# Kernel tuning notes

Hardware: AMD Instinct MI355X
Metric: run time of the kernel (lower is better)

## Reference

```python
import jax, jax.numpy as jnp
import numpy as np

B, N, R = 2, 64, 16
D = 64      # node_dim_in
H = 256     # hidden_dim
EOUT = 64   # edge_dim_out
PSTEP = 2


def _lin_init(key, fi, fo):
    k1, k2 = jax.random.split(key)
    s = 1.0 / np.sqrt(fi)
    W = jax.random.uniform(k1, (fi, fo), minval=-s, maxval=s, dtype=jnp.float32)
    b = jax.random.uniform(k2, (fo,), minval=-s, maxval=s, dtype=jnp.float32)
    return W, b


def setup_inputs() -> dict:
    key = jax.random.key(0)
    ks = jax.random.split(key, 11)
    node_rep = jax.random.normal(ks[0], (B, N, R, D), dtype=jnp.float32)
    ne_W, ne_b = _lin_init(ks[1], D, H)          # node_encoder
    ee_W, ee_b = _lin_init(ks[2], 2 * D, H)      # edge_encoder (edge_rep is None)
    np_W1, np_b1 = _lin_init(ks[3], 3 * H, H)    # node_propagator
    np_W2, np_b2 = _lin_init(ks[4], H, H)
    ep0_W1, ep0_b1 = _lin_init(ks[5], 3 * H, H)  # edge_propagators[0]
    ep0_W2, ep0_b2 = _lin_init(ks[6], H, H)
    ep1_W1, ep1_b1 = _lin_init(ks[7], 3 * H, H)  # edge_propagators[1]
    ep1_W2, ep1_b2 = _lin_init(ks[8], H, H)
    pr_W1, pr_b1 = _lin_init(ks[9], 2 * H, H)    # edge_predictor
    pr_W2, pr_b2 = _lin_init(ks[10], H, EOUT)
    return dict(node_rep=node_rep, ne_W=ne_W, ne_b=ne_b, ee_W=ee_W, ee_b=ee_b,
                np_W1=np_W1, np_b1=np_b1, np_W2=np_W2, np_b2=np_b2,
                ep0_W1=ep0_W1, ep0_b1=ep0_b1, ep0_W2=ep0_W2, ep0_b2=ep0_b2,
                ep1_W1=ep1_W1, ep1_b1=ep1_b1, ep1_W2=ep1_W2, ep1_b2=ep1_b2,
                pr_W1=pr_W1, pr_b1=pr_b1, pr_W2=pr_W2, pr_b2=pr_b2)


def _propnet(node_rep, ne_W, ne_b, ee_W, ee_b, np_W1, np_b1, np_W2, np_b2,
             ep_params, pr_W1, pr_b1, pr_W2, pr_b2):
    relu = jax.nn.relu
    # node encoder: [B,N,R,H]
    node_enc = relu(node_rep @ ne_W + ne_b)
    # edge encoder on cat(node_rep_r, node_rep_s): split the weight instead of
    # materializing the [B,N,N,R,2D] repeated-concat tensor (same math).
    # receiver varies over axis 1, sender over axis 2.
    edge_enc = relu(node_rep[:, :, None] @ ee_W[:D]
                    + node_rep[:, None, :] @ ee_W[D:] + ee_b)  # [B,N,N,R,H]
    node_effect = node_enc
    edge_effect = edge_enc
    for (W1, b1, W2, b2) in ep_params:
        # edge propagator on cat(effect_r, effect_s, edge_effect)
        h = relu(node_effect[:, :, None] @ W1[:H]
                 + node_effect[:, None, :] @ W1[H:2 * H]
                 + edge_effect @ W1[2 * H:] + b1)
        edge_effect = relu(h @ W2 + b2)                 # [B,N,N,R,H]
        agg = edge_effect.sum(axis=2)                   # sum over senders -> [B,N,R,H]
        g = relu(node_enc @ np_W1[:H]
                 + node_effect @ np_W1[H:2 * H]
                 + agg @ np_W1[2 * H:] + np_b1)
        node_effect = relu(g @ np_W2 + np_b2)
    # edge predictor on cat(edge_effect, edge_enc) -> split weight
    p = relu(edge_effect @ pr_W1[:H] + edge_enc @ pr_W1[H:] + pr_b1)
    edge_pred = p @ pr_W2 + pr_b2                       # [B,N,N,R,EOUT]
    return edge_pred


def reference(node_rep, ne_W, ne_b, ee_W, ee_b, np_W1, np_b1, np_W2, np_b2,
              ep0_W1, ep0_b1, ep0_W2, ep0_b2, ep1_W1, ep1_b1, ep1_W2, ep1_b2,
              pr_W1, pr_b1, pr_W2, pr_b2):
    ep_params = [(ep0_W1, ep0_b1, ep0_W2, ep0_b2), (ep1_W1, ep1_b1, ep1_W2, ep1_b2)]
    return _propnet(node_rep, ne_W, ne_b, ee_W, ee_b, np_W1, np_b1, np_W2, np_b2,
                    ep_params, pr_W1, pr_b1, pr_W2, pr_b2)
```

## Files before the change

### kernel.cpp

```cpp
#include <hip/hip_runtime.h>
#include <hip/hip_bf16.h>


typedef __attribute__((ext_vector_type(8))) short short8;
typedef __attribute__((ext_vector_type(4))) float f32x4;
typedef __attribute__((ext_vector_type(2))) unsigned int u32x2;

#define DI __device__ __forceinline__

constexpr size_t WF_SZ = 131072;
constexpr size_t OFF_NEW  = 14 * WF_SZ;
constexpr size_t OFF_EE1  = OFF_NEW + 32768;
constexpr size_t OFF_EE2  = OFF_EE1 + 32768;
constexpr size_t OFF_PW2  = OFF_EE2 + 32768;
constexpr size_t OFF_NENC = OFF_PW2 + 32768;
constexpr size_t OFF_X1   = OFF_NENC + (size_t)2048 * 256 * 2;
constexpr size_t SM = (size_t)2048 * 256 * 4;
constexpr size_t OFF_X2   = OFF_X1 + SM;
constexpr size_t OFF_E1   = OFF_X2 + SM;
constexpr size_t OFF_E2I  = OFF_E1 + SM;
constexpr size_t OFF_NE1  = OFF_E2I + 32 * 32768;
constexpr size_t OFF_AGG  = OFF_NE1 + SM;
constexpr size_t OFF_IMG  = OFF_AGG + 2 * SM;

DI unsigned short f2bf(float f) {
    unsigned u = __builtin_bit_cast(unsigned, f);
    u += 0x7fffu + ((u >> 16) & 1u);
    return (unsigned short)(u >> 16);
}
DI float bf2f(unsigned short s) {
    unsigned u = (unsigned)s << 16;
    return __builtin_bit_cast(float, u);
}

DI int kmap(int g, int e) { return 4 * g + (e & 3) + ((e >> 2) << 4); }

DI void dma16(const void* g, void* l) {
    __builtin_amdgcn_global_load_lds((const __attribute__((address_space(1))) void*)g,
                                     (__attribute__((address_space(3))) void*)l, 16, 0, 0);
}

__global__ __launch_bounds__(64) void kconv(const float* ep0W1, const float* ep0W2,
                                            const float* ep1W1, const float* ep1W2,
                                            const float* prW1, const float* prW2,
                                            const float* npW1, const float* npW2,
                                            const float* neW, const float* eeW,
                                            unsigned short* wsu)
{
    int bid = blockIdx.x, l = threadIdx.x;
    const float* src; unsigned short* dst; int NT = 16, ld = 256, f;
    if (bid < 1792) {
        int m = bid >> 7; f = bid & 127;
        switch (m) {
            case 0:  src = ep0W1 + 512 * 256; break;
            case 1:  src = ep0W2;             break;
            case 2:  src = ep1W1 + 512 * 256; break;
            case 3:  src = ep1W2;             break;
            case 4:  src = prW1;              break;
            case 5:  src = prW1 + 256 * 256;  break;
            case 6:  src = ep0W1;             break;
            case 7:  src = ep0W1 + 256 * 256; break;
            case 8:  src = npW1 + 256 * 256;  break;
            case 9:  src = npW1 + 512 * 256;  break;
            case 10: src = npW1;              break;
            case 11: src = npW2;              break;
            case 12: src = ep1W1;             break;
            default: src = ep1W1 + 256 * 256; break;
        }
        dst = wsu + (size_t)m * (WF_SZ / 2);
    } else if (bid < 1888) {
        int m = (bid - 1792) >> 5; f = (bid - 1792) & 31;
        src = (m == 0) ? neW : (m == 1) ? eeW : eeW + 64 * 256;
        dst = wsu + ((m == 0) ? OFF_NEW : (m == 1) ? OFF_EE1 : OFF_EE2) / 2;
    } else {
        f = bid - 1888; NT = 4; ld = 64; src = prW2; dst = wsu + OFF_PW2 / 2;
    }
    int kt = f / NT, nt = f % NT;
    int g = l >> 4, c = nt * 16 + (l & 15);
    unsigned short* o = dst + (size_t)((kt * NT + nt) * 64 + l) * 8;
#pragma unroll
    for (int e = 0; e < 8; ++e) {
        int k = 32 * kt + kmap(g, e);
        o[e] = f2bf(src[(size_t)k * ld + c]);
    }
}

template <int LDB>
DI short8 load_afrag(const unsigned char* lds, int row, int kt, int g) {
    int sw = (row & 7) << 4;
    int kb = 64 * kt + 8 * g;
    union { short8 s; u32x2 u[2]; } u_;
    u_.u[0] = *(const u32x2*)(lds + row * LDB + (kb ^ sw));
    u_.u[1] = *(const u32x2*)(lds + row * LDB + ((kb + 32) ^ sw));
    return u_.s;
}

template <int MI>
DI void zero_acc(f32x4 (&acc)[MI][4]) {
#pragma unroll
    for (int mi = 0; mi < MI; ++mi)
#pragma unroll
        for (int ni = 0; ni < 4; ++ni) acc[mi][ni] = (f32x4){0.f, 0.f, 0.f, 0.f};
}

template <int MI, int KT, int LDB>
DI void gemm_tile(const unsigned char* lds, const unsigned short* Wf,
                  f32x4 (&acc)[MI][4], int wv, int l) {
    const int g = l >> 4, l15 = l & 15;
    for (int kt = 0; kt < KT; ++kt) {
        short8 af[MI];
#pragma unroll
        for (int mi = 0; mi < MI; ++mi) af[mi] = load_afrag<LDB>(lds, 16 * mi + l15, kt, g);
        short8 bf[4];
#pragma unroll
        for (int ni = 0; ni < 4; ++ni)
            bf[ni] = *(const short8*)(Wf + (size_t)((kt * 16 + 4 * wv + ni) * 64 + l) * 8);
#pragma unroll
        for (int ni = 0; ni < 4; ++ni)
#pragma unroll
            for (int mi = 0; mi < MI; ++mi)
                acc[mi][ni] = __builtin_amdgcn_mfma_f32_16x16x32_bf16(af[mi], bf[ni], acc[mi][ni], 0, 0, 0);
    }
}

template <int MI>
DI void store_tile_f32(float* dst, int r0, f32x4 (&acc)[MI][4], int wv, int l) {
    int g = l >> 4, l15 = l & 15;
#pragma unroll
    for (int ni = 0; ni < 4; ++ni) {
        int col = 64 * wv + 16 * ni + l15;
#pragma unroll
        for (int mi = 0; mi < MI; ++mi)
#pragma unroll
            for (int q = 0; q < 4; ++q)
                dst[(size_t)(r0 + 16 * mi + 4 * g + q) * 256 + col] = acc[mi][ni][q];
    }
}

template <int MI>
DI void store_tile_bias(float* dst, const float* bias, int r0, f32x4 (&acc)[MI][4], int wv, int l) {
    int g = l >> 4, l15 = l & 15;
#pragma unroll
    for (int ni = 0; ni < 4; ++ni) {
        int col = 64 * wv + 16 * ni + l15;
        float bb = bias[col];
#pragma unroll
        for (int mi = 0; mi < MI; ++mi)
#pragma unroll
            for (int q = 0; q < 4; ++q)
                dst[(size_t)(r0 + 16 * mi + 4 * g + q) * 256 + col] = acc[mi][ni][q] + bb;
    }
}

template <int MI>
DI void store_E2img(unsigned char* E2img, int r0, f32x4 (&acc)[MI][4], int wv, int l) {
    int g = l >> 4, l15 = l & 15;
#pragma unroll
    for (int ni = 0; ni < 4; ++ni) {
        int col = 64 * wv + 16 * ni + l15;
#pragma unroll
        for (int mi = 0; mi < MI; ++mi)
#pragma unroll
            for (int q = 0; q < 4; ++q) {
                int nr = r0 + 16 * mi + 4 * g + q;
                int b = nr >> 10, j = (nr >> 4) & 63, r = nr & 15;
                size_t byte = (size_t)(b * 16 + r) * 32768 + ((j * 512 + col * 2) ^ ((j & 7) << 4));
                *(unsigned short*)(E2img + byte) = f2bf(acc[mi][ni][q]);
            }
    }
}

__global__ __launch_bounds__(256) void knode12(const float* node_rep, const float* neb,
        const float* ep0b1,
        const unsigned short* neWf, const unsigned short* eeW1f, const unsigned short* eeW2f,
        const unsigned short* E1wf, const unsigned short* E2wf, const unsigned short* NE1wf,
        unsigned short* node_enc, float* X1, float* X2, float* E1b, unsigned char* E2img, float* NE1)
{
    __shared__ __align__(16) unsigned char ldsA[32 * 128];
    __shared__ __align__(16) unsigned char ldsB[32 * 512];
    const int r0 = blockIdx.x * 32, tid = threadIdx.x;
    {
        int row = tid >> 3, c0 = (tid & 7) * 8;
        const float* src = node_rep + (size_t)(r0 + row) * 64 + c0;
        union { short8 s; unsigned short u[8]; } v;
#pragma unroll
        for (int e = 0; e < 8; ++e) v.u[e] = f2bf(src[e]);
        *(short8*)&ldsA[row * 128 + ((c0 * 2) ^ ((row & 7) << 4))] = v.s;
    }
    __syncthreads();
    const int l = tid & 63, wv = tid >> 6, g = l >> 4, l15 = l & 15;
    f32x4 acc[2][4];
    zero_acc(acc);
    gemm_tile<2, 2, 128>(ldsA, neWf, acc, wv, l);
#pragma unroll
    for (int ni = 0; ni < 4; ++ni) {
        int col = 64 * wv + 16 * ni + l15;
        float bb = neb[col];
#pragma unroll
        for (int mi = 0; mi < 2; ++mi)
#pragma unroll
            for (int q = 0; q < 4; ++q) {
                int row = 16 * mi + 4 * g + q;
                unsigned short bv = f2bf(fmaxf(acc[mi][ni][q] + bb, 0.f));
                *(unsigned short*)&ldsB[row * 512 + ((col * 2) ^ ((row & 7) << 4))] = bv;
                node_enc[(size_t)(r0 + row) * 256 + col] = bv;
            }
    }
    zero_acc(acc);
    gemm_tile<2, 2, 128>(ldsA, eeW1f, acc, wv, l);
    store_tile_f32<2>(X1, r0, acc, wv, l);
    zero_acc(acc);
    gemm_tile<2, 2, 128>(ldsA, eeW2f, acc, wv, l);
    store_tile_f32<2>(X2, r0, acc, wv, l);
    __syncthreads();
    zero_acc(acc);
    gemm_tile<2, 8, 512>(ldsB, E1wf, acc, wv, l);
    store_tile_bias<2>(E1b, ep0b1, r0, acc, wv, l);
    zero_acc(acc);
    gemm_tile<2, 8, 512>(ldsB, E2wf, acc, wv, l);
    store_E2img<2>(E2img, r0, acc, wv, l);
    zero_acc(acc);
    gemm_tile<2, 8, 512>(ldsB, NE1wf, acc, wv, l);
    store_tile_f32<2>(NE1, r0, acc, wv, l);
}

__global__ __launch_bounds__(256) void knode3(const unsigned short* node_enc, const float* agg,
        const float* NE1, const float* npb1, const float* npb2, const float* ep1b1,
        const unsigned short* NE2wf, const unsigned short* NAGGwf, const unsigned short* npW2f,
        const unsigned short* ep1Awf, const unsigned short* ep1Bwf,
        float* E1b, unsigned char* E2img)
{
    __shared__ __align__(16) unsigned char ldsA[32 * 512];
    __shared__ __align__(16) unsigned char ldsB[32 * 512];
    const int r0 = blockIdx.x * 32, tid = threadIdx.x;
    {
        int row = tid >> 3, cbase = (tid & 7) * 32;
        int sw = (row & 7) << 4;
#pragma unroll
        for (int cc = 0; cc < 2; ++cc) {
            int c0 = cbase + cc * 16;
            short8 lo = *(const short8*)(node_enc + (size_t)(r0 + row) * 256 + c0);
            short8 hi = *(const short8*)(node_enc + (size_t)(r0 + row) * 256 + c0 + 8);
            *(short8*)&ldsA[row * 512 + ((c0 * 2) ^ sw)] = lo;
            *(short8*)&ldsA[row * 512 + ((c0 * 2 + 16) ^ sw)] = hi;
            union { short8 s; unsigned short u[8]; } v0, v1;
            const float* aA = agg + (size_t)(r0 + row) * 256 + c0;
            const float* aB = aA + (size_t)2048 * 256;
#pragma unroll
            for (int e = 0; e < 8; ++e) {
                v0.u[e] = f2bf(aA[e] + aB[e]);
                v1.u[e] = f2bf(aA[8 + e] + aB[8 + e]);
            }
            *(short8*)&ldsB[row * 512 + ((c0 * 2) ^ sw)] = v0.s;
            *(short8*)&ldsB[row * 512 + ((c0 * 2 + 16) ^ sw)] = v1.s;
        }
    }
    __syncthreads();
    const int l = tid & 63, wv = tid >> 6, g = l >> 4, l15 = l & 15;
    f32x4 acc[2][4];
    zero_acc(acc);
    gemm_tile<2, 8, 512>(ldsA, NE2wf, acc, wv, l);
    gemm_tile<2, 8, 512>(ldsB, NAGGwf, acc, wv, l);
    __syncthreads();
#pragma unroll
    for (int ni = 0; ni < 4; ++ni) {
        int col = 64 * wv + 16 * ni + l15;
        float bb = npb1[col];
#pragma unroll
        for (int mi = 0; mi < 2; ++mi)
#pragma unroll
            for (int q = 0; q < 4; ++q) {
                int row = 16 * mi + 4 * g + q;
                float v = fmaxf(acc[mi][ni][q] + NE1[(size_t)(r0 + row) * 256 + col] + bb, 0.f);
                *(unsigned short*)&ldsA[row * 512 + ((col * 2) ^ ((row & 7) << 4))] = f2bf(v);
            }
    }
    __syncthreads();
    zero_acc(acc);
    gemm_tile<2, 8, 512>(ldsA, npW2f, acc, wv, l);
    __syncthreads();
#pragma unroll
    for (int ni = 0; ni < 4; ++ni) {
        int col = 64 * wv + 16 * ni + l15;
        float bb = npb2[col];
#pragma unroll
        for (int mi = 0; mi < 2; ++mi)
#pragma unroll
            for (int q = 0; q < 4; ++q) {
                int row = 16 * mi + 4 * g + q;
                *(unsigned short*)&ldsB[row * 512 + ((col * 2) ^ ((row & 7) << 4))] =
                    f2bf(fmaxf(acc[mi][ni][q] + bb, 0.f));
            }
    }
    __syncthreads();
    zero_acc(acc);
    gemm_tile<2, 8, 512>(ldsB, ep1Awf, acc, wv, l);
    store_tile_bias<2>(E1b, ep1b1, r0, acc, wv, l);
    zero_acc(acc);
    gemm_tile<2, 8, 512>(ldsB, ep1Bwf, acc, wv, l);
    store_E2img<2>(E2img, r0, acc, wv, l);
}

__global__ __launch_bounds__(256, 2) void kstep1(const float* X1, const float* X2, const float* eeb,
                                                 const float* E1b, const unsigned char* E2img,
                                                 const float* b2,
                                                 const unsigned short* WfA, const unsigned short* WfB,
                                                 unsigned char* img, float* agg)
{
    __shared__ __align__(16) unsigned char T[32 * 512];
    __shared__ __align__(16) unsigned char L2e[32 * 512];
    const int bb = blockIdx.x, tid = threadIdx.x;
    const int bir = bb >> 1, half = bb & 1;
    const int b = bir >> 10, r = bir & 15;
    const int l = tid & 63, wv = tid >> 6, g = l >> 4, l15 = l & 15;

    {
        const unsigned char* src = E2img + (size_t)(b * 16 + r) * 32768 + (size_t)half * 16384;
#pragma unroll
        for (int p = 0; p < 4; ++p) {
            int chunk = wv * 4 + p;
            dma16(src + chunk * 1024 + l * 16, &L2e[chunk * 1024]);
        }
    }
    {
        int rlo = tid >> 5;
        int c0 = (tid & 31) * 8;
        for (int p = 0; p < 4; ++p) {
            int row = p * 8 + rlo;
            union { short8 s; unsigned short u[8]; } v;
            int nrj = b * 1024 + (half * 32 + row) * 16 + r;
#pragma unroll
            for (int e = 0; e < 8; ++e) {
                float x = X1[(size_t)bir * 256 + c0 + e] + X2[(size_t)nrj * 256 + c0 + e] + eeb[c0 + e];
                v.u[e] = f2bf(fmaxf(x, 0.f));
            }
            *(short8*)&T[row * 512 + ((c0 * 2) ^ ((row & 7) << 4))] = v.s;
        }
    }
    __syncthreads();

    f32x4 acc[2][4];
    zero_acc(acc);
    gemm_tile<2, 8, 512>(T, WfA, acc, wv, l);
    __syncthreads();
#pragma unroll
    for (int ni = 0; ni < 4; ++ni) {
        int col = 64 * wv + 16 * ni + l15;
        float e1b = E1b[(size_t)bir * 256 + col];
#pragma unroll
        for (int mi = 0; mi < 2; ++mi)
#pragma unroll
            for (int q = 0; q < 4; ++q) {
                int row = 16 * mi + 4 * g + q;
                float e2 = bf2f(*(const unsigned short*)&L2e[row * 512 + ((col * 2) ^ ((row & 7) << 4))]);
                float h = fmaxf(acc[mi][ni][q] + e1b + e2, 0.f);
                *(unsigned short*)&T[row * 512 + ((col * 2) ^ ((row & 7) << 4))] = f2bf(h);
                acc[mi][ni][q] = 0.f;
            }
    }
    __syncthreads();
    gemm_tile<2, 8, 512>(T, WfB, acc, wv, l);
    unsigned short* out16 = (unsigned short*)(img + (size_t)bb * 16384);
#pragma unroll
    for (int ni = 0; ni < 4; ++ni) {
        int col = 64 * wv + 16 * ni + l15;
        float bb2 = b2[col];
        float s = 0.f;
#pragma unroll
        for (int mi = 0; mi < 2; ++mi)
#pragma unroll
            for (int q = 0; q < 4; ++q) {
                int row = 16 * mi + 4 * g + q;
                float e = fmaxf(acc[mi][ni][q] + bb2, 0.f);
                out16[(row * 512 + ((col * 2) ^ ((row & 7) << 4))) >> 1] = f2bf(e);
                s += e;
            }
        s += __shfl_xor(s, 16);
        s += __shfl_xor(s, 32);
        if (l < 16) agg[((size_t)half * 2048 + bir) * 256 + 64 * wv + 16 * ni + l] = s;
    }
}

__global__ __launch_bounds__(256, 2) void kstep2pred(const float* X1, const float* X2, const float* eeb,
        const float* E1b, const unsigned char* E2img, const float* b2,
        const unsigned short* WfA, const unsigned short* WfB,
        const unsigned short* WfPA, const unsigned short* WfPB, const unsigned short* WfP2,
        const float* prb1, const float* prb2,
        const unsigned char* img, float* out)
{
    __shared__ __align__(16) unsigned char T[32 * 512];
    __shared__ __align__(16) unsigned char L2e[32 * 512];
    const int bb = blockIdx.x, tid = threadIdx.x;
    const int bir = bb >> 1, half = bb & 1;
    const int b = bir >> 10, r = bir & 15;
    const int ebase = (bir >> 4) * 1024 + r;
    const int l = tid & 63, wv = tid >> 6, g = l >> 4, l15 = l & 15;

    {
        const unsigned char* src = img + (size_t)bb * 16384;
        const unsigned char* srcE = E2img + (size_t)(b * 16 + r) * 32768 + (size_t)half * 16384;
#pragma unroll
        for (int p = 0; p < 4; ++p) {
            int chunk = wv * 4 + p;
            dma16(src + chunk * 1024 + l * 16, &T[chunk * 1024]);
            dma16(srcE + chunk * 1024 + l * 16, &L2e[chunk * 1024]);
        }
    }
    __syncthreads();

    f32x4 acc[2][4];
    zero_acc(acc);
    gemm_tile<2, 8, 512>(T, WfA, acc, wv, l);
    __syncthreads();
#pragma unroll
    for (int ni = 0; ni < 4; ++ni) {
        int col = 64 * wv + 16 * ni + l15;
        float e1b = E1b[(size_t)bir * 256 + col];
#pragma unroll
        for (int mi = 0; mi < 2; ++mi)
#pragma unroll
            for (int q = 0; q < 4; ++q) {
                int row = 16 * mi + 4 * g + q;
                float e2 = bf2f(*(const unsigned short*)&L2e[row * 512 + ((col * 2) ^ ((row & 7) << 4))]);
                float h = fmaxf(acc[mi][ni][q] + e1b + e2, 0.f);
                *(unsigned short*)&T[row * 512 + ((col * 2) ^ ((row & 7) << 4))] = f2bf(h);
                acc[mi][ni][q] = 0.f;
            }
    }
    __syncthreads();
    gemm_tile<2, 8, 512>(T, WfB, acc, wv, l);
    __syncthreads();
#pragma unroll
    for (int ni = 0; ni < 4; ++ni) {
        int col = 64 * wv + 16 * ni + l15;
        float bb2 = b2[col];
#pragma unroll
        for (int mi = 0; mi < 2; ++mi)
#pragma unroll
            for (int q = 0; q < 4; ++q) {
                int row = 16 * mi + 4 * g + q;
                *(unsigned short*)&T[row * 512 + ((col * 2) ^ ((row & 7) << 4))] =
                    f2bf(fmaxf(acc[mi][ni][q] + bb2, 0.f));
            }
    }
    __syncthreads();
    zero_acc(acc);
    gemm_tile<2, 8, 512>(T, WfPA, acc, wv, l);
    __syncthreads();
    {
        int rlo = tid >> 5;
        int c0 = (tid & 31) * 8;
        for (int p = 0; p < 4; ++p) {
            int row = p * 8 + rlo;
            union { short8 s; unsigned short u[8]; } v;
            int nrj = b * 1024 + (half * 32 + row) * 16 + r;
#pragma unroll
            for (int e = 0; e < 8; ++e) {
                float x = X1[(size_t)bir * 256 + c0 + e] + X2[(size_t)nrj * 256 + c0 + e] + eeb[c0 + e];
                v.u[e] = f2bf(fmaxf(x, 0.f));
            }
            *(short8*)&T[row * 512 + ((c0 * 2) ^ ((row & 7) << 4))] = v.s;
        }
    }
    __syncthreads();
    gemm_tile<2, 8, 512>(T, WfPB, acc, wv, l);
    __syncthreads();
#pragma unroll
    for (int ni = 0; ni < 4; ++ni) {
        int col = 64 * wv + 16 * ni + l15;
        float pb = prb1[col];
#pragma unroll
        for (int mi = 0; mi < 2; ++mi)
#pragma unroll
            for (int q = 0; q < 4; ++q) {
                int row = 16 * mi + 4 * g + q;
                float p = fmaxf(acc[mi][ni][q] + pb, 0.f);
                *(unsigned short*)&T[row * 512 + ((col * 2) ^ ((row & 7) << 4))] = f2bf(p);
            }
    }
    __syncthreads();
    f32x4 acc3[2];
#pragma unroll
    for (int mi = 0; mi < 2; ++mi) acc3[mi] = (f32x4){0.f, 0.f, 0.f, 0.f};
    for (int kt = 0; kt < 8; ++kt) {
        short8 bf = *(const short8*)(WfP2 + (size_t)((kt * 4 + wv) * 64 + l) * 8);
#pragma unroll
        for (int mi = 0; mi < 2; ++mi) {
            short8 af = load_afrag<512>(T, 16 * mi + l15, kt, g);
            acc3[mi] = __builtin_amdgcn_mfma_f32_16x16x32_bf16(af, bf, acc3[mi], 0, 0, 0);
        }
    }
    int colo = 16 * wv + l15;
    float pb2 = prb2[colo];
#pragma unroll
    for (int mi = 0; mi < 2; ++mi)
#pragma unroll
        for (int q = 0; q < 4; ++q) {
            int row = 16 * mi + 4 * g + q;
            out[(size_t)(ebase + (half * 32 + row) * 16) * 64 + colo] = acc3[mi][q] + pb2;
        }
}

extern "C" void kernel_launch(void* const* d_in, const int* in_sizes, int n_in,
                              void* d_out, int out_size, void* d_ws, size_t ws_size,
                              hipStream_t stream)
{
    (void)in_sizes; (void)n_in; (void)out_size; (void)ws_size;
    const float* node_rep = (const float*)d_in[0];
    const float* neW   = (const float*)d_in[1];
    const float* neb   = (const float*)d_in[2];
    const float* eeW   = (const float*)d_in[3];
    const float* eeb   = (const float*)d_in[4];
    const float* npW1  = (const float*)d_in[5];
    const float* npb1  = (const float*)d_in[6];
    const float* npW2  = (const float*)d_in[7];
    const float* npb2  = (const float*)d_in[8];
    const float* ep0W1 = (const float*)d_in[9];
    const float* ep0b1 = (const float*)d_in[10];
    const float* ep0W2 = (const float*)d_in[11];
    const float* ep0b2 = (const float*)d_in[12];
    const float* ep1W1 = (const float*)d_in[13];
    const float* ep1b1 = (const float*)d_in[14];
    const float* ep1W2 = (const float*)d_in[15];
    const float* ep1b2 = (const float*)d_in[16];
    const float* prW1  = (const float*)d_in[17];
    const float* prb1  = (const float*)d_in[18];
    const float* prW2  = (const float*)d_in[19];
    const float* prb2  = (const float*)d_in[20];

    char* ws = (char*)d_ws;
    unsigned short* wsu = (unsigned short*)ws;
    auto wfull = [&](int i) { return (const unsigned short*)(ws + (size_t)i * WF_SZ); };
    unsigned short* node_enc = (unsigned short*)(ws + OFF_NENC);
    float* X1   = (float*)(ws + OFF_X1);
    float* X2   = (float*)(ws + OFF_X2);
    float* E1b  = (float*)(ws + OFF_E1);
    unsigned char* E2img = (unsigned char*)(ws + OFF_E2I);
    float* NE1  = (float*)(ws + OFF_NE1);
    float* agg  = (float*)(ws + OFF_AGG);
    unsigned char* img = (unsigned char*)(ws + OFF_IMG);
    const unsigned short* neWf  = (const unsigned short*)(ws + OFF_NEW);
    const unsigned short* eeW1f = (const unsigned short*)(ws + OFF_EE1);
    const unsigned short* eeW2f = (const unsigned short*)(ws + OFF_EE2);
    const unsigned short* prW2f = (const unsigned short*)(ws + OFF_PW2);

    kconv<<<dim3(1920), dim3(64), 0, stream>>>(ep0W1, ep0W2, ep1W1, ep1W2, prW1, prW2,
                                               npW1, npW2, neW, eeW, wsu);
    knode12<<<dim3(64), dim3(256), 0, stream>>>(node_rep, neb, ep0b1, neWf, eeW1f, eeW2f,
                                                wfull(6), wfull(7), wfull(10),
                                                node_enc, X1, X2, E1b, E2img, NE1);
    kstep1<<<dim3(4096), dim3(256), 0, stream>>>(X1, X2, eeb, E1b, E2img, ep0b2,
                                                 wfull(0), wfull(1), img, agg);
    knode3<<<dim3(64), dim3(256), 0, stream>>>(node_enc, agg, NE1, npb1, npb2, ep1b1,
                                               wfull(8), wfull(9), wfull(11),
                                               wfull(12), wfull(13), E1b, E2img);
    kstep2pred<<<dim3(4096), dim3(256), 0, stream>>>(X1, X2, eeb, E1b, E2img, ep1b2,
                                                     wfull(2), wfull(3), wfull(4), wfull(5),
                                                     prW2f, prb1, prb2, img, (float*)d_out);
}
```

Before: 344.5 us.

## Load sender edge term from fp32 global into registers and double-buffer LDS

The sender-side E2 projection is now kept as an fp32 row-major buffer instead of a swizzled bf16 image. The edge kernels read it directly into registers per accumulator element, with no LDS DMA staging. A second LDS buffer (U) alternates with T so several __syncthreads barriers between GEMM phases can be dropped. The cost is twice the bytes for E2, uncoalesced scattered global loads, and extra register pressure from 36 prefetched floats under a 2-blocks-per-SM launch bound.

```diff
diff --git a/kernel.cpp b/kernel.cpp
--- a/kernel.cpp
+++ b/kernel.cpp
@@ -18,8 +18,8 @@
 constexpr size_t SM = (size_t)2048 * 256 * 4;
 constexpr size_t OFF_X2   = OFF_X1 + SM;
 constexpr size_t OFF_E1   = OFF_X2 + SM;
-constexpr size_t OFF_E2I  = OFF_E1 + SM;
-constexpr size_t OFF_NE1  = OFF_E2I + 32 * 32768;
+constexpr size_t OFF_E2   = OFF_E1 + SM;
+constexpr size_t OFF_NE1  = OFF_E2 + SM;
 constexpr size_t OFF_AGG  = OFF_NE1 + SM;
 constexpr size_t OFF_IMG  = OFF_AGG + 2 * SM;
 
@@ -27,10 +27,6 @@
     unsigned u = __builtin_bit_cast(unsigned, f);
     u += 0x7fffu + ((u >> 16) & 1u);
     return (unsigned short)(u >> 16);
-}
-DI float bf2f(unsigned short s) {
-    unsigned u = (unsigned)s << 16;
-    return __builtin_bit_cast(float, u);
 }
 
 DI int kmap(int g, int e) { return 4 * g + (e & 3) + ((e >> 2) << 4); }
@@ -152,29 +148,11 @@
     }
 }
 
-template <int MI>
-DI void store_E2img(unsigned char* E2img, int r0, f32x4 (&acc)[MI][4], int wv, int l) {
-    int g = l >> 4, l15 = l & 15;
-#pragma unroll
-    for (int ni = 0; ni < 4; ++ni) {
-        int col = 64 * wv + 16 * ni + l15;
-#pragma unroll
-        for (int mi = 0; mi < MI; ++mi)
-#pragma unroll
-            for (int q = 0; q < 4; ++q) {
-                int nr = r0 + 16 * mi + 4 * g + q;
-                int b = nr >> 10, j = (nr >> 4) & 63, r = nr & 15;
-                size_t byte = (size_t)(b * 16 + r) * 32768 + ((j * 512 + col * 2) ^ ((j & 7) << 4));
-                *(unsigned short*)(E2img + byte) = f2bf(acc[mi][ni][q]);
-            }
-    }
-}
-
 __global__ __launch_bounds__(256) void knode12(const float* node_rep, const float* neb,
         const float* ep0b1,
         const unsigned short* neWf, const unsigned short* eeW1f, const unsigned short* eeW2f,
         const unsigned short* E1wf, const unsigned short* E2wf, const unsigned short* NE1wf,
-        unsigned short* node_enc, float* X1, float* X2, float* E1b, unsigned char* E2img, float* NE1)
+        unsigned short* node_enc, float* X1, float* X2, float* E1b, float* E2, float* NE1)
 {
     __shared__ __align__(16) unsigned char ldsA[32 * 128];
     __shared__ __align__(16) unsigned char ldsB[32 * 512];
@@ -218,7 +196,7 @@
     store_tile_bias<2>(E1b, ep0b1, r0, acc, wv, l);
     zero_acc(acc);
     gemm_tile<2, 8, 512>(ldsB, E2wf, acc, wv, l);
-    store_E2img<2>(E2img, r0, acc, wv, l);
+    store_tile_f32<2>(E2, r0, acc, wv, l);
     zero_acc(acc);
     gemm_tile<2, 8, 512>(ldsB, NE1wf, acc, wv, l);
     store_tile_f32<2>(NE1, r0, acc, wv, l);
@@ -228,7 +206,7 @@
         const float* NE1, const float* npb1, const float* npb2, const float* ep1b1,
         const unsigned short* NE2wf, const unsigned short* NAGGwf, const unsigned short* npW2f,
         const unsigned short* ep1Awf, const unsigned short* ep1Bwf,
-        float* E1b, unsigned char* E2img)
+        float* E1b, float* E2)
 {
     __shared__ __align__(16) unsigned char ldsA[32 * 512];
     __shared__ __align__(16) unsigned char ldsB[32 * 512];
@@ -298,33 +276,23 @@
     store_tile_bias<2>(E1b, ep1b1, r0, acc, wv, l);
     zero_acc(acc);
     gemm_tile<2, 8, 512>(ldsB, ep1Bwf, acc, wv, l);
-    store_E2img<2>(E2img, r0, acc, wv, l);
+    store_tile_f32<2>(E2, r0, acc, wv, l);
 }
 
 __global__ __launch_bounds__(256, 2) void kstep1(const float* X1, const float* X2, const float* eeb,
-                                                 const float* E1b, const unsigned char* E2img,
-                                                 const float* b2,
+                                                 const float* E1b, const float* E2, const float* b2,
                                                  const unsigned short* WfA, const unsigned short* WfB,
                                                  unsigned char* img, float* agg)
 {
     __shared__ __align__(16) unsigned char T[32 * 512];
-    __shared__ __align__(16) unsigned char L2e[32 * 512];
+    __shared__ __align__(16) unsigned char U[32 * 512];
     const int bb = blockIdx.x, tid = threadIdx.x;
     const int bir = bb >> 1, half = bb & 1;
     const int b = bir >> 10, r = bir & 15;
     const int l = tid & 63, wv = tid >> 6, g = l >> 4, l15 = l & 15;
 
     {
-        const unsigned char* src = E2img + (size_t)(b * 16 + r) * 32768 + (size_t)half * 16384;
-#pragma unroll
-        for (int p = 0; p < 4; ++p) {
-            int chunk = wv * 4 + p;
-            dma16(src + chunk * 1024 + l * 16, &L2e[chunk * 1024]);
-        }
-    }
-    {
-        int rlo = tid >> 5;
-        int c0 = (tid & 31) * 8;
+        int rlo = tid >> 5, c0 = (tid & 31) * 8;
         for (int p = 0; p < 4; ++p) {
             int row = p * 8 + rlo;
             union { short8 s; unsigned short u[8]; } v;
@@ -339,27 +307,37 @@
     }
     __syncthreads();
 
+    float e2p[4][8], e1p[4];
+#pragma unroll
+    for (int ni = 0; ni < 4; ++ni) {
+        int col = 64 * wv + 16 * ni + l15;
+        e1p[ni] = E1b[(size_t)bir * 256 + col];
+#pragma unroll
+        for (int mi = 0; mi < 2; ++mi)
+#pragma unroll
+            for (int q = 0; q < 4; ++q) {
+                int row = 16 * mi + 4 * g + q;
+                e2p[ni][mi * 4 + q] = E2[(size_t)(b * 1024 + (half * 32 + row) * 16 + r) * 256 + col];
+            }
+    }
     f32x4 acc[2][4];
     zero_acc(acc);
     gemm_tile<2, 8, 512>(T, WfA, acc, wv, l);
-    __syncthreads();
-#pragma unroll
-    for (int ni = 0; ni < 4; ++ni) {
-        int col = 64 * wv + 16 * ni + l15;
-        float e1b = E1b[(size_t)bir * 256 + col];
-#pragma unroll
-        for (int mi = 0; mi < 2; ++mi)
-#pragma unroll
-            for (int q = 0; q < 4; ++q) {
-                int row = 16 * mi + 4 * g + q;
-                float e2 = bf2f(*(const unsigned short*)&L2e[row * 512 + ((col * 2) ^ ((row & 7) << 4))]);
-                float h = fmaxf(acc[mi][ni][q] + e1b + e2, 0.f);
-                *(unsigned short*)&T[row * 512 + ((col * 2) ^ ((row & 7) << 4))] = f2bf(h);
+#pragma unroll
+    for (int ni = 0; ni < 4; ++ni) {
+        int col = 64 * wv + 16 * ni + l15;
+#pragma unroll
+        for (int mi = 0; mi < 2; ++mi)
+#pragma unroll
+            for (int q = 0; q < 4; ++q) {
+                int row = 16 * mi + 4 * g + q;
+                float h = fmaxf(acc[mi][ni][q] + e1p[ni] + e2p[ni][mi * 4 + q], 0.f);
+                *(unsigned short*)&U[row * 512 + ((col * 2) ^ ((row & 7) << 4))] = f2bf(h);
                 acc[mi][ni][q] = 0.f;
             }
     }
     __syncthreads();
-    gemm_tile<2, 8, 512>(T, WfB, acc, wv, l);
+    gemm_tile<2, 8, 512>(U, WfB, acc, wv, l);
     unsigned short* out16 = (unsigned short*)(img + (size_t)bb * 16384);
 #pragma unroll
     for (int ni = 0; ni < 4; ++ni) {
@@ -382,14 +360,14 @@
 }
 
 __global__ __launch_bounds__(256, 2) void kstep2pred(const float* X1, const float* X2, const float* eeb,
-        const float* E1b, const unsigned char* E2img, const float* b2,
+        const float* E1b, const float* E2, const float* b2,
         const unsigned short* WfA, const unsigned short* WfB,
         const unsigned short* WfPA, const unsigned short* WfPB, const unsigned short* WfP2,
         const float* prb1, const float* prb2,
         const unsigned char* img, float* out)
 {
     __shared__ __align__(16) unsigned char T[32 * 512];
-    __shared__ __align__(16) unsigned char L2e[32 * 512];
+    __shared__ __align__(16) unsigned char U[32 * 512];
     const int bb = blockIdx.x, tid = threadIdx.x;
     const int bir = bb >> 1, half = bb & 1;
     const int b = bir >> 10, r = bir & 15;
@@ -398,38 +376,45 @@
 
     {
         const unsigned char* src = img + (size_t)bb * 16384;
-        const unsigned char* srcE = E2img + (size_t)(b * 16 + r) * 32768 + (size_t)half * 16384;
 #pragma unroll
         for (int p = 0; p < 4; ++p) {
             int chunk = wv * 4 + p;
             dma16(src + chunk * 1024 + l * 16, &T[chunk * 1024]);
-            dma16(srcE + chunk * 1024 + l * 16, &L2e[chunk * 1024]);
-        }
+        }
+    }
+    float e2p[4][8], e1p[4];
+#pragma unroll
+    for (int ni = 0; ni < 4; ++ni) {
+        int col = 64 * wv + 16 * ni + l15;
+        e1p[ni] = E1b[(size_t)bir * 256 + col];
+#pragma unroll
+        for (int mi = 0; mi < 2; ++mi)
+#pragma unroll
+            for (int q = 0; q < 4; ++q) {
+                int row = 16 * mi + 4 * g + q;
+                e2p[ni][mi * 4 + q] = E2[(size_t)(b * 1024 + (half * 32 + row) * 16 + r) * 256 + col];
+            }
     }
     __syncthreads();
 
     f32x4 acc[2][4];
     zero_acc(acc);
     gemm_tile<2, 8, 512>(T, WfA, acc, wv, l);
-    __syncthreads();
-#pragma unroll
-    for (int ni = 0; ni < 4; ++ni) {
-        int col = 64 * wv + 16 * ni + l15;
-        float e1b = E1b[(size_t)bir * 256 + col];
-#pragma unroll
-        for (int mi = 0; mi < 2; ++mi)
-#pragma unroll
-            for (int q = 0; q < 4; ++q) {
-                int row = 16 * mi + 4 * g + q;
-                float e2 = bf2f(*(const unsigned short*)&L2e[row * 512 + ((col * 2) ^ ((row & 7) << 4))]);
-                float h = fmaxf(acc[mi][ni][q] + e1b + e2, 0.f);
-                *(unsigned short*)&T[row * 512 + ((col * 2) ^ ((row & 7) << 4))] = f2bf(h);
+#pragma unroll
+    for (int ni = 0; ni < 4; ++ni) {
+        int col = 64 * wv + 16 * ni + l15;
+#pragma unroll
+        for (int mi = 0; mi < 2; ++mi)
+#pragma unroll
+            for (int q = 0; q < 4; ++q) {
+                int row = 16 * mi + 4 * g + q;
+                float h = fmaxf(acc[mi][ni][q] + e1p[ni] + e2p[ni][mi * 4 + q], 0.f);
+                *(unsigned short*)&U[row * 512 + ((col * 2) ^ ((row & 7) << 4))] = f2bf(h);
                 acc[mi][ni][q] = 0.f;
             }
     }
     __syncthreads();
-    gemm_tile<2, 8, 512>(T, WfB, acc, wv, l);
-    __syncthreads();
+    gemm_tile<2, 8, 512>(U, WfB, acc, wv, l);
 #pragma unroll
     for (int ni = 0; ni < 4; ++ni) {
         int col = 64 * wv + 16 * ni + l15;
@@ -441,15 +426,13 @@
                 int row = 16 * mi + 4 * g + q;
                 *(unsigned short*)&T[row * 512 + ((col * 2) ^ ((row & 7) << 4))] =
                     f2bf(fmaxf(acc[mi][ni][q] + bb2, 0.f));
-            }
-    }
-    __syncthreads();
-    zero_acc(acc);
+                acc[mi][ni][q] = 0.f;
+            }
+    }
+    __syncthreads();
     gemm_tile<2, 8, 512>(T, WfPA, acc, wv, l);
-    __syncthreads();
     {
-        int rlo = tid >> 5;
-        int c0 = (tid & 31) * 8;
+        int rlo = tid >> 5, c0 = (tid & 31) * 8;
         for (int p = 0; p < 4; ++p) {
             int row = p * 8 + rlo;
             union { short8 s; unsigned short u[8]; } v;
@@ -459,12 +442,11 @@
                 float x = X1[(size_t)bir * 256 + c0 + e] + X2[(size_t)nrj * 256 + c0 + e] + eeb[c0 + e];
                 v.u[e] = f2bf(fmaxf(x, 0.f));
             }
-            *(short8*)&T[row * 512 + ((c0 * 2) ^ ((row & 7) << 4))] = v.s;
-        }
-    }
-    __syncthreads();
-    gemm_tile<2, 8, 512>(T, WfPB, acc, wv, l);
-    __syncthreads();
+            *(short8*)&U[row * 512 + ((c0 * 2) ^ ((row & 7) << 4))] = v.s;
+        }
+    }
+    __syncthreads();
+    gemm_tile<2, 8, 512>(U, WfPB, acc, wv, l);
 #pragma unroll
     for (int ni = 0; ni < 4; ++ni) {
         int col = 64 * wv + 16 * ni + l15;
@@ -535,7 +517,7 @@
     float* X1   = (float*)(ws + OFF_X1);
     float* X2   = (float*)(ws + OFF_X2);
     float* E1b  = (float*)(ws + OFF_E1);
-    unsigned char* E2img = (unsigned char*)(ws + OFF_E2I);
+    float* E2   = (float*)(ws + OFF_E2);
     float* NE1  = (float*)(ws + OFF_NE1);
     float* agg  = (float*)(ws + OFF_AGG);
     unsigned char* img = (unsigned char*)(ws + OFF_IMG);
@@ -548,13 +530,13 @@
                                                npW1, npW2, neW, eeW, wsu);
     knode12<<<dim3(64), dim3(256), 0, stream>>>(node_rep, neb, ep0b1, neWf, eeW1f, eeW2f,
                                                 wfull(6), wfull(7), wfull(10),
-                                                node_enc, X1, X2, E1b, E2img, NE1);
-    kstep1<<<dim3(4096), dim3(256), 0, stream>>>(X1, X2, eeb, E1b, E2img, ep0b2,
+                                                node_enc, X1, X2, E1b, E2, NE1);
+    kstep1<<<dim3(4096), dim3(256), 0, stream>>>(X1, X2, eeb, E1b, E2, ep0b2,
                                                  wfull(0), wfull(1), img, agg);
     knode3<<<dim3(64), dim3(256), 0, stream>>>(node_enc, agg, NE1, npb1, npb2, ep1b1,
                                                wfull(8), wfull(9), wfull(11),
-                                               wfull(12), wfull(13), E1b, E2img);
-    kstep2pred<<<dim3(4096), dim3(256), 0, stream>>>(X1, X2, eeb, E1b, E2img, ep1b2,
+                                               wfull(12), wfull(13), E1b, E2);
+    kstep2pred<<<dim3(4096), dim3(256), 0, stream>>>(X1, X2, eeb, E1b, E2, ep1b2,
                                                      wfull(2), wfull(3), wfull(4), wfull(5),
                                                      prW2f, prb1, prb2, img, (float*)d_out);
 }
```

New measurement: 342.6 us. About the same (-0.5%).
